# Performance work log

Measured on AMD Instinct MI355X. Metric: run time of the kernel, lower is better.

Reference implementation:

```python
import jax, jax.numpy as jnp
import numpy as np

N_NODES = 50000
N_EDGES = 800000
DIMS = [100, 512, 256, 128, 200]  # input -> conv1 -> conv2 -> conv3 -> conv4


def setup_inputs() -> dict:
    key = jax.random.key(0)
    ks = jax.random.split(key, 2 + 4)
    x = jax.random.normal(ks[0], (N_NODES, DIMS[0]), dtype=jnp.float32)
    edge_index = jax.random.randint(ks[1], (2, N_EDGES), 0, N_NODES, dtype=jnp.int64)
    inp = {"x": x, "edge_index": edge_index}
    for i in range(4):
        fan_in = DIMS[i]
        W = jax.random.normal(ks[2 + i], (DIMS[i], DIMS[i + 1]), dtype=jnp.float32) * (1.0 / np.sqrt(fan_in)).astype(np.float32)
        b = jnp.zeros((DIMS[i + 1],), dtype=jnp.float32)
        inp[f"W{i + 1}"] = W
        inp[f"b{i + 1}"] = b
    return inp


def _gcn_layer(x, row, col, norm, W, b, n):
    # PyG GCNConv: linear transform first, then normalized scatter-add, then bias.
    h = x @ W                           # [N, out]
    msg = h[row] * norm[:, None]        # [E+N, out] gather + edge scale
    agg = jax.ops.segment_sum(msg, col, num_segments=n)  # scatter-add to targets
    return agg + b


def reference(x, edge_index, W1, b1, W2, b2, W3, b3, W4, b4):
    n = x.shape[0]
    loop = jnp.arange(n, dtype=edge_index.dtype)
    row = jnp.concatenate([edge_index[0], loop])  # sources (with self-loops)
    col = jnp.concatenate([edge_index[1], loop])  # targets (with self-loops)
    deg = jax.ops.segment_sum(jnp.ones_like(col, dtype=x.dtype), col, num_segments=n)
    dinv = jnp.where(deg > 0, jax.lax.rsqrt(deg), 0.0)
    norm = dinv[row] * dinv[col]  # symmetric D^{-1/2}(A+I)D^{-1/2} edge weights

    out = jax.nn.relu(_gcn_layer(x, row, col, norm, W1, b1, n))
    out = jax.nn.relu(_gcn_layer(out, row, col, norm, W2, b2, n))
    out = jax.nn.relu(_gcn_layer(out, row, col, norm, W3, b3, n))
    out = jax.nn.relu(_gcn_layer(out, row, col, norm, W4, b4, n))
    return jnp.mean(out, axis=0, keepdims=True)  # [1, 200]
```

## Files before the change

kernel.cpp:

```cpp
#include <hip/hip_runtime.h>
#include <hip/hip_bf16.h>


#define NN 50000
#define NE 800000

typedef __attribute__((ext_vector_type(8))) _Float16 f16x8;
typedef __attribute__((ext_vector_type(4))) float floatx4;
typedef __attribute__((ext_vector_type(2))) float floatx2;

union U16x8 {
    uint4 u4;
    f16x8 h;
    _Float16 e[8];
};

__device__ __forceinline__ void dec16(const unsigned char* p, float* f) {
    uint4 v = *(const uint4*)p;
    unsigned w[4] = {v.x, v.y, v.z, v.w};
#pragma unroll
    for (int k = 0; k < 4; k++) {
        floatx2 lo = __builtin_amdgcn_cvt_pk_f32_fp8(w[k], false);
        floatx2 hi = __builtin_amdgcn_cvt_pk_f32_fp8(w[k], true);
        f[k * 4 + 0] = lo[0];
        f[k * 4 + 1] = lo[1];
        f[k * 4 + 2] = hi[0];
        f[k * 4 + 3] = hi[1];
    }
}

__device__ __forceinline__ uint4 enc16(const float* f) {
    uint4 r;
    unsigned w;
    w = __builtin_amdgcn_cvt_pk_fp8_f32(f[0], f[1], 0, false);
    w = __builtin_amdgcn_cvt_pk_fp8_f32(f[2], f[3], (int)w, true);
    r.x = w;
    w = __builtin_amdgcn_cvt_pk_fp8_f32(f[4], f[5], 0, false);
    w = __builtin_amdgcn_cvt_pk_fp8_f32(f[6], f[7], (int)w, true);
    r.y = w;
    w = __builtin_amdgcn_cvt_pk_fp8_f32(f[8], f[9], 0, false);
    w = __builtin_amdgcn_cvt_pk_fp8_f32(f[10], f[11], (int)w, true);
    r.z = w;
    w = __builtin_amdgcn_cvt_pk_fp8_f32(f[12], f[13], 0, false);
    w = __builtin_amdgcn_cvt_pk_fp8_f32(f[14], f[15], (int)w, true);
    r.w = w;
    return r;
}

__device__ __forceinline__ uint4 dec8_f16(uint2 v) {
    floatx2 f0 = __builtin_amdgcn_cvt_pk_f32_fp8(v.x, false);
    floatx2 f1 = __builtin_amdgcn_cvt_pk_f32_fp8(v.x, true);
    floatx2 f2 = __builtin_amdgcn_cvt_pk_f32_fp8(v.y, false);
    floatx2 f3 = __builtin_amdgcn_cvt_pk_f32_fp8(v.y, true);
    U16x8 o;
    o.e[0] = (_Float16)f0[0]; o.e[1] = (_Float16)f0[1];
    o.e[2] = (_Float16)f1[0]; o.e[3] = (_Float16)f1[1];
    o.e[4] = (_Float16)f2[0]; o.e[5] = (_Float16)f2[1];
    o.e[6] = (_Float16)f3[0]; o.e[7] = (_Float16)f3[1];
    return o.u4;
}

__global__ __launch_bounds__(256) void zero_detect_kernel(
    const unsigned* __restrict__ ei, int* __restrict__ flag,
    unsigned* __restrict__ cnt, unsigned* __restrict__ fillc,
    float* __restrict__ out) {
    int tid = blockIdx.x * 256 + threadIdx.x;
    if (tid < NN) {
        cnt[tid] = 0u;
        fillc[tid] = 0u;
    }
    if (blockIdx.x == 0) {
        if (threadIdx.x < 200) out[threadIdx.x] = 0.f;
        unsigned w = ei[2 * threadIdx.x + 1];
        unsigned long long any = __ballot(w != 0);
        if (threadIdx.x == 0) *flag = (any == 0ull) ? 1 : 0;
    }
}

__global__ __launch_bounds__(256) void count_kernel(const void* ei,
                                                    const int* __restrict__ flag,
                                                    unsigned* __restrict__ cnt) {
    int base = (blockIdx.x * 256 + threadIdx.x) * 4;
    if (base >= NE) return;
    int c[4];
    if (*flag) {
        const long long* p = (const long long*)ei + NE;
#pragma unroll
        for (int i = 0; i < 4; i++) c[i] = (int)p[base + i];
    } else {
        const int* p = (const int*)ei + NE;
#pragma unroll
        for (int i = 0; i < 4; i++) c[i] = p[base + i];
    }
#pragma unroll
    for (int i = 0; i < 4; i++) atomicAdd(&cnt[c[i]], 1u);
}

__global__ __launch_bounds__(256) void scan1_kernel(const unsigned* __restrict__ cnt,
                                                    int* __restrict__ off,
                                                    int* __restrict__ bsum,
                                                    float* __restrict__ dinv) {
    __shared__ int ws[4];
    int b = blockIdx.x, t = threadIdx.x;
    int base = b * 1024 + t * 4;
    int v[4];
    int s = 0;
#pragma unroll
    for (int i = 0; i < 4; i++) {
        int val = 0;
        if (base + i < NN) {
            val = (int)cnt[base + i];
            dinv[base + i] = rsqrtf((float)(val + 1));
        }
        v[i] = s;
        s += val;
    }
    int lane = t & 63, wv = t >> 6;
    int x = s;
    for (int d = 1; d < 64; d <<= 1) {
        int y = __shfl_up(x, d, 64);
        if (lane >= d) x += y;
    }
    if (lane == 63) ws[wv] = x;
    __syncthreads();
    int wpre = 0;
#pragma unroll
    for (int i = 0; i < 4; i++)
        if (i < wv) wpre += ws[i];
    int texcl = x - s + wpre;
#pragma unroll
    for (int i = 0; i < 4; i++)
        if (base + i < NN) off[base + i] = texcl + v[i];
    if (t == 255) bsum[b] = texcl + s;
}

__global__ void scan2_kernel(int* bsum, int nb) {
    int t = threadIdx.x;
    int v = (t < nb) ? bsum[t] : 0;
    int x = v;
    for (int d = 1; d < 64; d <<= 1) {
        int y = __shfl_up(x, d, 64);
        if (t >= d) x += y;
    }
    if (t < nb) bsum[t] = x - v;
}

__global__ __launch_bounds__(256) void scan3_kernel(int* __restrict__ off,
                                                    const int* __restrict__ bsum) {
    int b = blockIdx.x;
    int add = bsum[b];
    int base = b * 1024 + threadIdx.x * 4;
#pragma unroll
    for (int i = 0; i < 4; i++)
        if (base + i < NN) off[base + i] += add;
    if (b == 0 && threadIdx.x == 0) off[NN] = NE;
}

__global__ __launch_bounds__(256) void fill_kernel(
    const void* ei, const int* __restrict__ flag, const int* __restrict__ off,
    unsigned* __restrict__ fillc, const float* __restrict__ dinv,
    int2* __restrict__ ep) {
    int base = (blockIdx.x * 256 + threadIdx.x) * 4;
    if (base >= NE) return;
    int r[4], c[4];
    if (*flag) {
        const long long* p = (const long long*)ei;
#pragma unroll
        for (int i = 0; i < 4; i++) {
            r[i] = (int)p[base + i];
            c[i] = (int)p[NE + base + i];
        }
    } else {
        const int* p = (const int*)ei;
#pragma unroll
        for (int i = 0; i < 4; i++) {
            r[i] = p[base + i];
            c[i] = p[NE + base + i];
        }
    }
    int pos[4];
#pragma unroll
    for (int i = 0; i < 4; i++)
        pos[i] = off[c[i]] + (int)atomicAdd(&fillc[c[i]], 1u);
#pragma unroll
    for (int i = 0; i < 4; i++) {
        int2 v;
        v.x = r[i];
        v.y = __float_as_int(dinv[r[i]] * dinv[c[i]]);
        ep[pos[i]] = v;
    }
}

__global__ __launch_bounds__(256) void xwcast_kernel(
    const float* __restrict__ x, unsigned char* __restrict__ xb,
    const float* __restrict__ W1, const float* __restrict__ W2,
    const float* __restrict__ W3, const float* __restrict__ W4,
    _Float16* __restrict__ w1t, _Float16* __restrict__ w2t,
    _Float16* __restrict__ w3t, _Float16* __restrict__ w4t) {
    int bx = blockIdx.x, t = threadIdx.x;
    if (bx < 1563) {
        int tid = bx * 256 + t;
        int node = tid >> 3, sub = tid & 7;
        if (node >= NN) return;
        int base = sub * 16;
        float f[16];
#pragma unroll
        for (int i = 0; i < 16; i++) {
            int c = base + i;
            f[i] = (c < 100) ? x[(size_t)node * 100 + c] : 0.f;
        }
        *(uint4*)(xb + (size_t)node * 128 + base) = enc16(f);
        return;
    }
    int b = bx - 1563;
    const float* W;
    _Float16* Wt;
    int K, N, Kpad, tid;
    if (b < 256)      { W = W1; Wt = w1t; K = 100; N = 512; Kpad = 128; tid = b * 256 + t; }
    else if (b < 768) { W = W2; Wt = w2t; K = 512; N = 256; Kpad = 512; tid = (b - 256) * 256 + t; }
    else if (b < 896) { W = W3; Wt = w3t; K = 256; N = 128; Kpad = 256; tid = (b - 768) * 256 + t; }
    else              { W = W4; Wt = w4t; K = 128; N = 200; Kpad = 128; tid = (b - 896) * 256 + t; }
    int n = tid / Kpad, k = tid - n * Kpad;
    float v = (k < K && n < N) ? W[(size_t)k * N + n] : 0.f;
    Wt[tid] = (_Float16)v;
}

template <int D, int BR>
__global__ __launch_bounds__(256) void agg_kernel(
    const unsigned char* __restrict__ H, const int* __restrict__ off,
    const int2* __restrict__ ep, const float* __restrict__ dinv,
    const float* __restrict__ bias, unsigned char* __restrict__ O) {
    constexpr int LPN = D / 16;
    int tid = blockIdx.x * 256 + threadIdx.x;
    int node = tid / LPN;
    int sub = tid % LPN;
    if (node >= NN) return;
    int s = off[node], e = off[node + 1];
    float dc = dinv[node];
    float selfw = dc * dc;
    const int base = sub * 16;
    const unsigned char* __restrict__ Hb = H + base;
    float acc[16], t0[16], t1[16];
    dec16(Hb + (size_t)node * D, t0);
#pragma unroll
    for (int i = 0; i < 16; i++) acc[i] = selfw * t0[i];
    int j = s;
    for (; j + 2 <= e; j += 2) {
        int2 q0 = ep[j];
        int2 q1 = ep[j + 1];
        dec16(Hb + (size_t)q0.x * D, t0);
        dec16(Hb + (size_t)q1.x * D, t1);
        float w0 = __int_as_float(q0.y);
        float w1 = __int_as_float(q1.y);
#pragma unroll
        for (int i = 0; i < 16; i++) acc[i] = fmaf(w0, t0[i], acc[i]);
#pragma unroll
        for (int i = 0; i < 16; i++) acc[i] = fmaf(w1, t1[i], acc[i]);
    }
    if (j < e) {
        int2 q0 = ep[j];
        dec16(Hb + (size_t)q0.x * D, t0);
        float w0 = __int_as_float(q0.y);
#pragma unroll
        for (int i = 0; i < 16; i++) acc[i] = fmaf(w0, t0[i], acc[i]);
    }
    if (BR) {
#pragma unroll
        for (int i = 0; i < 16; i++) acc[i] = fmaxf(acc[i] + bias[base + i], 0.f);
    }
    *(uint4*)(O + (size_t)node * D + base) = enc16(acc);
}

template <int EPI>
__global__ __launch_bounds__(256) void gemm_kernel(
    const unsigned char* __restrict__ A, const _Float16* __restrict__ B,
    const float* __restrict__ bias, unsigned char* __restrict__ Cb,
    float* __restrict__ outmean, int M, int K, int N) {
    __shared__ _Float16 Asl[128 * 40];
    __shared__ _Float16 Bsl[128 * 40];
    __shared__ float red[128];
    const int m0 = blockIdx.y * 128;
    const int n0 = blockIdx.x * 128;
    const int t = threadIdx.x;
    const int lane = t & 63, w = t >> 6;
    const int wm = (w >> 1) * 64, wn = (w & 1) * 64;
    const int r16 = lane & 15, quad = lane >> 4;

    floatx4 acc[4][4];
    const floatx4 fz = {0.f, 0.f, 0.f, 0.f};
#pragma unroll
    for (int i = 0; i < 4; i++)
#pragma unroll
        for (int j = 0; j < 4; j++) acc[i][j] = fz;

    for (int kc = 0; kc < K; kc += 32) {
        __syncthreads();
#pragma unroll
        for (int i = 0; i < 2; i++) {
            int seg = t + 256 * i;
            int row = seg >> 2, k8 = (seg & 3) * 8;
            int gm = m0 + row;
            if (gm > M - 1) gm = M - 1;
            uint2 av = *(const uint2*)(A + (size_t)gm * K + kc + k8);
            *(uint4*)(Asl + row * 40 + k8) = dec8_f16(av);
            int gn = n0 + row;
            *(uint4*)(Bsl + row * 40 + k8) = *(const uint4*)(B + (size_t)gn * K + kc + k8);
        }
        __syncthreads();
        f16x8 af[4], bf[4];
#pragma unroll
        for (int i = 0; i < 4; i++)
            af[i] = *(const f16x8*)(Asl + (wm + i * 16 + r16) * 40 + quad * 8);
#pragma unroll
        for (int j = 0; j < 4; j++)
            bf[j] = *(const f16x8*)(Bsl + (wn + j * 16 + r16) * 40 + quad * 8);
#pragma unroll
        for (int i = 0; i < 4; i++)
#pragma unroll
            for (int j = 0; j < 4; j++)
                acc[i][j] = __builtin_amdgcn_mfma_f32_16x16x32_f16(af[i], bf[j], acc[i][j], 0, 0, 0);
    }

    if (EPI == 2) {
        if (t < 128) red[t] = 0.f;
        __syncthreads();
#pragma unroll
        for (int j = 0; j < 4; j++) {
            int col = n0 + wn + j * 16 + r16;
            float s = 0.f;
            if (col < N) {
                float bv = bias[col];
#pragma unroll
                for (int i = 0; i < 4; i++)
#pragma unroll
                    for (int r = 0; r < 4; r++) {
                        int m = m0 + wm + i * 16 + quad * 4 + r;
                        if (m < M) s += fmaxf(acc[i][j][r] + bv, 0.f);
                    }
            }
            atomicAdd(&red[wn + j * 16 + r16], s);
        }
        __syncthreads();
        if (t < 128) {
            int col = n0 + t;
            if (col < N) atomicAdd(outmean + col, red[t] * (1.0f / (float)NN));
        }
    } else {
#pragma unroll
        for (int i = 0; i < 4; i++)
#pragma unroll
            for (int r = 0; r < 4; r++) {
                int m = m0 + wm + i * 16 + quad * 4 + r;
                if (m >= M) continue;
#pragma unroll
                for (int j = 0; j < 4; j++) {
                    int col = n0 + wn + j * 16 + r16;
                    float v = acc[i][j][r];
                    if (EPI == 1) v = fmaxf(v + bias[col], 0.f);
                    unsigned pk = __builtin_amdgcn_cvt_pk_fp8_f32(v, v, 0, false);
                    Cb[(size_t)m * N + col] = (unsigned char)(pk & 0xffu);
                }
            }
    }
}

extern "C" void kernel_launch(void* const* d_in, const int* in_sizes, int n_in,
                              void* d_out, int out_size, void* d_ws, size_t ws_size,
                              hipStream_t stream) {
    const float* x  = (const float*)d_in[0];
    const void*  ei = d_in[1];
    const float* W1 = (const float*)d_in[2];
    const float* b1 = (const float*)d_in[3];
    const float* W2 = (const float*)d_in[4];
    const float* b2 = (const float*)d_in[5];
    const float* W3 = (const float*)d_in[6];
    const float* b3 = (const float*)d_in[7];
    const float* W4 = (const float*)d_in[8];
    const float* b4 = (const float*)d_in[9];
    float* out = (float*)d_out;

    char* ws = (char*)d_ws;
    size_t o = 0;
    auto alloc = [&](size_t bytes) -> void* {
        void* p = ws + o;
        o += (bytes + 255) & ~(size_t)255;
        return p;
    };
    int*      flag  = (int*)alloc(4);
    unsigned* cnt   = (unsigned*)alloc((size_t)NN * 4);
    int*      off   = (int*)alloc((size_t)(NN + 1) * 4);
    unsigned* fillc = (unsigned*)alloc((size_t)NN * 4);
    float*    dinv  = (float*)alloc((size_t)NN * 4);
    int2*     ep    = (int2*)alloc((size_t)NE * 8);
    _Float16* w1t = (_Float16*)alloc((size_t)512 * 128 * 2);
    _Float16* w2t = (_Float16*)alloc((size_t)256 * 512 * 2);
    _Float16* w3t = (_Float16*)alloc((size_t)128 * 256 * 2);
    _Float16* w4t = (_Float16*)alloc((size_t)256 * 128 * 2);
    int*      bsum  = (int*)alloc(256);
    unsigned char* xb  = (unsigned char*)alloc((size_t)NN * 128);
    unsigned char* A1b = (unsigned char*)alloc((size_t)NN * 128);
    unsigned char* H1b = (unsigned char*)alloc((size_t)NN * 512);
    unsigned char* t2b = (unsigned char*)alloc((size_t)NN * 256);
    unsigned char* H2b = (unsigned char*)alloc((size_t)NN * 256);
    unsigned char* t3b = (unsigned char*)alloc((size_t)NN * 128);
    unsigned char* h3b = (unsigned char*)alloc((size_t)NN * 128);
    unsigned char* A4b = (unsigned char*)alloc((size_t)NN * 128);

    const int EB4 = (NE / 4 + 255) / 256;
    const int NB1 = (NN + 1023) / 1024;
    const int ZB = (NN + 255) / 256;

    zero_detect_kernel<<<ZB, 256, 0, stream>>>((const unsigned*)ei, flag, cnt, fillc, out);
    count_kernel<<<EB4, 256, 0, stream>>>(ei, flag, cnt);
    scan1_kernel<<<NB1, 256, 0, stream>>>(cnt, off, bsum, dinv);
    scan2_kernel<<<1, 64, 0, stream>>>(bsum, NB1);
    scan3_kernel<<<NB1, 256, 0, stream>>>(off, bsum);
    fill_kernel<<<EB4, 256, 0, stream>>>(ei, flag, off, fillc, dinv, ep);
    xwcast_kernel<<<1563 + 1024, 256, 0, stream>>>(x, xb, W1, W2, W3, W4, w1t, w2t, w3t, w4t);

    const int MB = (NN + 127) / 128;
    const int AB128 = (NN * 8 + 255) / 256;
    const int AB256 = (NN * 16 + 255) / 256;

    agg_kernel<128, 0><<<AB128, 256, 0, stream>>>(xb, off, ep, dinv, nullptr, A1b);
    gemm_kernel<1><<<dim3(4, MB), 256, 0, stream>>>(A1b, w1t, b1, H1b, nullptr, NN, 128, 512);
    gemm_kernel<0><<<dim3(2, MB), 256, 0, stream>>>(H1b, w2t, nullptr, t2b, nullptr, NN, 512, 256);
    agg_kernel<256, 1><<<AB256, 256, 0, stream>>>(t2b, off, ep, dinv, b2, H2b);
    gemm_kernel<0><<<dim3(1, MB), 256, 0, stream>>>(H2b, w3t, nullptr, t3b, nullptr, NN, 256, 128);
    agg_kernel<128, 1><<<AB128, 256, 0, stream>>>(t3b, off, ep, dinv, b3, h3b);
    agg_kernel<128, 0><<<AB128, 256, 0, stream>>>(h3b, off, ep, dinv, nullptr, A4b);
    gemm_kernel<2><<<dim3(2, MB), 256, 0, stream>>>(A4b, w4t, b4, nullptr, out, NN, 128, 200);
}
```

Before: 356.4 us.

## Partition count/fill by target range and store only source index in CSR

Count and fill kernels now use 1024 blocks split into 8 node-range partitions. Each block scans a strided slice of edges and only does atomics for targets in its partition, which localises atomic traffic and CSR writes to a range that may stay cache-resident (e.g. per-XCD on MI355X). The edge payload shrinks from int2 (source, weight) to a plain int source, so the aggregation kernels recompute each weight as dinv[src]*dinv[dst] with an extra gather instead of loading a precomputed weight. In exchange, every edge index is read by all 8 partitions, and aggregation does more random dinv loads.

```diff
diff --git a/kernel.cpp b/kernel.cpp
--- a/kernel.cpp
+++ b/kernel.cpp
@@ -4,6 +4,8 @@
 
 #define NN 50000
 #define NE 800000
+#define NPART 8
+#define PRANGE (NN / NPART)
 
 typedef __attribute__((ext_vector_type(8))) _Float16 f16x8;
 typedef __attribute__((ext_vector_type(4))) float floatx4;
@@ -80,20 +82,16 @@
 __global__ __launch_bounds__(256) void count_kernel(const void* ei,
                                                     const int* __restrict__ flag,
                                                     unsigned* __restrict__ cnt) {
-    int base = (blockIdx.x * 256 + threadIdx.x) * 4;
-    if (base >= NE) return;
-    int c[4];
-    if (*flag) {
-        const long long* p = (const long long*)ei + NE;
-#pragma unroll
-        for (int i = 0; i < 4; i++) c[i] = (int)p[base + i];
-    } else {
-        const int* p = (const int*)ei + NE;
-#pragma unroll
-        for (int i = 0; i < 4; i++) c[i] = p[base + i];
-    }
-#pragma unroll
-    for (int i = 0; i < 4; i++) atomicAdd(&cnt[c[i]], 1u);
+    const int part = blockIdx.x & 7;
+    const int lo = part * PRANGE, hi = lo + PRANGE;
+    const int group = blockIdx.x >> 3;
+    const int f64 = *flag;
+    const long long* p64 = (const long long*)ei + NE;
+    const int* p32 = (const int*)ei + NE;
+    for (int e = group * 256 + threadIdx.x; e < NE; e += 128 * 256) {
+        int c = f64 ? (int)p64[e] : p32[e];
+        if (c >= lo && c < hi) atomicAdd(&cnt[c], 1u);
+    }
 }
 
 __global__ __launch_bounds__(256) void scan1_kernel(const unsigned* __restrict__ cnt,
@@ -158,36 +156,20 @@
 
 __global__ __launch_bounds__(256) void fill_kernel(
     const void* ei, const int* __restrict__ flag, const int* __restrict__ off,
-    unsigned* __restrict__ fillc, const float* __restrict__ dinv,
-    int2* __restrict__ ep) {
-    int base = (blockIdx.x * 256 + threadIdx.x) * 4;
-    if (base >= NE) return;
-    int r[4], c[4];
-    if (*flag) {
-        const long long* p = (const long long*)ei;
-#pragma unroll
-        for (int i = 0; i < 4; i++) {
-            r[i] = (int)p[base + i];
-            c[i] = (int)p[NE + base + i];
-        }
-    } else {
-        const int* p = (const int*)ei;
-#pragma unroll
-        for (int i = 0; i < 4; i++) {
-            r[i] = p[base + i];
-            c[i] = p[NE + base + i];
-        }
-    }
-    int pos[4];
-#pragma unroll
-    for (int i = 0; i < 4; i++)
-        pos[i] = off[c[i]] + (int)atomicAdd(&fillc[c[i]], 1u);
-#pragma unroll
-    for (int i = 0; i < 4; i++) {
-        int2 v;
-        v.x = r[i];
-        v.y = __float_as_int(dinv[r[i]] * dinv[c[i]]);
-        ep[pos[i]] = v;
+    unsigned* __restrict__ fillc, int* __restrict__ ep) {
+    const int part = blockIdx.x & 7;
+    const int lo = part * PRANGE, hi = lo + PRANGE;
+    const int group = blockIdx.x >> 3;
+    const int f64 = *flag;
+    const long long* p64 = (const long long*)ei;
+    const int* p32 = (const int*)ei;
+    for (int e = group * 256 + threadIdx.x; e < NE; e += 128 * 256) {
+        int c = f64 ? (int)p64[NE + e] : p32[NE + e];
+        if (c >= lo && c < hi) {
+            int r = f64 ? (int)p64[e] : p32[e];
+            int pos = off[c] + (int)atomicAdd(&fillc[c], 1u);
+            ep[pos] = r;
+        }
     }
 }
 
@@ -228,7 +210,7 @@
 template <int D, int BR>
 __global__ __launch_bounds__(256) void agg_kernel(
     const unsigned char* __restrict__ H, const int* __restrict__ off,
-    const int2* __restrict__ ep, const float* __restrict__ dinv,
+    const int* __restrict__ ep, const float* __restrict__ dinv,
     const float* __restrict__ bias, unsigned char* __restrict__ O) {
     constexpr int LPN = D / 16;
     int tid = blockIdx.x * 256 + threadIdx.x;
@@ -246,21 +228,21 @@
     for (int i = 0; i < 16; i++) acc[i] = selfw * t0[i];
     int j = s;
     for (; j + 2 <= e; j += 2) {
-        int2 q0 = ep[j];
-        int2 q1 = ep[j + 1];
-        dec16(Hb + (size_t)q0.x * D, t0);
-        dec16(Hb + (size_t)q1.x * D, t1);
-        float w0 = __int_as_float(q0.y);
-        float w1 = __int_as_float(q1.y);
+        int r0 = ep[j];
+        int r1 = ep[j + 1];
+        float w0 = dinv[r0] * dc;
+        float w1 = dinv[r1] * dc;
+        dec16(Hb + (size_t)r0 * D, t0);
+        dec16(Hb + (size_t)r1 * D, t1);
 #pragma unroll
         for (int i = 0; i < 16; i++) acc[i] = fmaf(w0, t0[i], acc[i]);
 #pragma unroll
         for (int i = 0; i < 16; i++) acc[i] = fmaf(w1, t1[i], acc[i]);
     }
     if (j < e) {
-        int2 q0 = ep[j];
-        dec16(Hb + (size_t)q0.x * D, t0);
-        float w0 = __int_as_float(q0.y);
+        int r0 = ep[j];
+        float w0 = dinv[r0] * dc;
+        dec16(Hb + (size_t)r0 * D, t0);
 #pragma unroll
         for (int i = 0; i < 16; i++) acc[i] = fmaf(w0, t0[i], acc[i]);
     }
@@ -391,7 +373,7 @@
     int*      off   = (int*)alloc((size_t)(NN + 1) * 4);
     unsigned* fillc = (unsigned*)alloc((size_t)NN * 4);
     float*    dinv  = (float*)alloc((size_t)NN * 4);
-    int2*     ep    = (int2*)alloc((size_t)NE * 8);
+    int*      ep    = (int*)alloc((size_t)NE * 4);
     _Float16* w1t = (_Float16*)alloc((size_t)512 * 128 * 2);
     _Float16* w2t = (_Float16*)alloc((size_t)256 * 512 * 2);
     _Float16* w3t = (_Float16*)alloc((size_t)128 * 256 * 2);
@@ -406,16 +388,16 @@
     unsigned char* h3b = (unsigned char*)alloc((size_t)NN * 128);
     unsigned char* A4b = (unsigned char*)alloc((size_t)NN * 128);
 
-    const int EB4 = (NE / 4 + 255) / 256;
     const int NB1 = (NN + 1023) / 1024;
     const int ZB = (NN + 255) / 256;
+    const int PB = 1024;
 
     zero_detect_kernel<<<ZB, 256, 0, stream>>>((const unsigned*)ei, flag, cnt, fillc, out);
-    count_kernel<<<EB4, 256, 0, stream>>>(ei, flag, cnt);
+    count_kernel<<<PB, 256, 0, stream>>>(ei, flag, cnt);
     scan1_kernel<<<NB1, 256, 0, stream>>>(cnt, off, bsum, dinv);
     scan2_kernel<<<1, 64, 0, stream>>>(bsum, NB1);
     scan3_kernel<<<NB1, 256, 0, stream>>>(off, bsum);
-    fill_kernel<<<EB4, 256, 0, stream>>>(ei, flag, off, fillc, dinv, ep);
+    fill_kernel<<<PB, 256, 0, stream>>>(ei, flag, off, fillc, ep);
     xwcast_kernel<<<1563 + 1024, 256, 0, stream>>>(x, xb, W1, W2, W3, W4, w1t, w2t, w3t, w4t);
 
     const int MB = (NN + 127) / 128;
```

Result: no change. 354.2 us (-0.6%).
